# Performance work log

Hardware: AMD Instinct MI355X
Metric: run time of the kernel (lower is better)

The kernel has to match this reference:

```python
import jax, jax.numpy as jnp
import numpy as np

UNITS = 1024
INPUT_SIZE = 1024


def setup_inputs() -> dict:
    key = jax.random.key(0)
    k1, k2, k3 = jax.random.split(key, 3)
    T, B = 512, 64
    inputs = jax.random.normal(k1, (T, B, INPUT_SIZE), dtype=jnp.float32)
    # xavier_uniform for kernel
    limit = float(np.sqrt(6.0 / (INPUT_SIZE + 4 * UNITS)))
    kernel = jax.random.uniform(k2, (INPUT_SIZE, 4 * UNITS), dtype=jnp.float32,
                                minval=-limit, maxval=limit)
    # orthogonal init for recurrent_kernel
    a = jax.random.normal(k3, (4 * UNITS, UNITS), dtype=jnp.float32)
    q, r = jnp.linalg.qr(a)
    q = q * jnp.sign(jnp.diagonal(r))[None, :]
    recurrent_kernel = q.T.astype(jnp.float32)  # [UNITS, 4*UNITS]
    bias = jnp.zeros((4 * UNITS,), dtype=jnp.float32)
    return {"inputs": inputs, "kernel": kernel,
            "recurrent_kernel": recurrent_kernel, "bias": bias}


def _lstm(inputs, kernel, recurrent_kernel, bias):
    T, B, _ = inputs.shape
    U = recurrent_kernel.shape[0]
    # Precompute input projection for all timesteps (same math, one big GEMM)
    xz = jnp.einsum('tbi,ij->tbj', inputs, kernel) + bias  # [T, B, 4U]

    def step(carry, xz_t):
        ht, ct = carry
        z = xz_t + ht @ recurrent_kernel  # [B, 4U]
        z_i, z_f, z_c, z_o = jnp.split(z, 4, axis=1)
        i = jax.nn.sigmoid(z_i)
        f = jax.nn.sigmoid(z_f)
        c_tilde = jnp.tanh(z_c)
        o = jax.nn.sigmoid(z_o)
        ct = f * ct + i * c_tilde
        ht = o * jnp.tanh(ct)
        return (ht, ct), ht

    h0 = jnp.zeros((B, U), dtype=inputs.dtype)
    c0 = jnp.zeros((B, U), dtype=inputs.dtype)
    (ht, ct), outputs = jax.lax.scan(step, (h0, c0), xz)
    return outputs, (ht, ct)


def reference(inputs, kernel, recurrent_kernel, bias):
    return _lstm(inputs, kernel, recurrent_kernel, bias)
```

## Files before the change

### kernel.cpp

```cpp
#include <hip/hip_runtime.h>

typedef __attribute__((ext_vector_type(8))) short short8;
typedef __attribute__((ext_vector_type(4))) float floatx4;

#define T_STEPS 512
#define OUT_HT_OFF 33554432ull
#define OUT_CT_OFF 33619968ull

#define WXH_OFF  0ull
#define WXL_OFF  (8ull << 20)
#define BAR_OFF  (16ull << 20)
#define WS_NEED  ((16ull << 20) + 4096)


static __device__ __forceinline__ unsigned short bf16_rne(float f) {
    union { float f; unsigned int u; } v; v.f = f;
    return (unsigned short)((v.u + 0x7FFFu + ((v.u >> 16) & 1u)) >> 16);
}
static __device__ __forceinline__ float bf16f(unsigned short u) {
    union { unsigned int u; float f; } v; v.u = ((unsigned int)u) << 16;
    return v.f;
}

__global__ void ws_sentinel(float* out) { out[threadIdx.x] = 2.0f; }

__global__ void __launch_bounds__(256) wsplit(const float* __restrict__ W,
                                              unsigned short* __restrict__ wxh,
                                              unsigned short* __restrict__ wxl) {
    __shared__ float tile[64][65];
    const int tx = threadIdx.x & 63;
    const int ty = threadIdx.x >> 6;
    const int cb = blockIdx.x * 64;
    const int kb = blockIdx.y * 64;
    #pragma unroll
    for (int i = 0; i < 16; ++i) {
        int kl = i * 4 + ty;
        tile[kl][tx] = W[(size_t)(kb + kl) * 4096 + cb + tx];
    }
    __syncthreads();
    #pragma unroll
    for (int i = 0; i < 16; ++i) {
        int cl = i * 4 + ty;
        float v = tile[tx][cl];
        unsigned short hi = bf16_rne(v);
        unsigned short lo = bf16_rne(v - bf16f(hi));
        wxh[(size_t)(cb + cl) * 1024 + kb + tx] = hi;
        wxl[(size_t)(cb + cl) * 1024 + kb + tx] = lo;
    }
}

static __device__ __forceinline__ void bar_arrive(unsigned* bar, int xcd, unsigned s) {
    unsigned old = __hip_atomic_fetch_add(bar + xcd * 32, 1u,
                      __ATOMIC_RELAXED, __HIP_MEMORY_SCOPE_AGENT);
    if (old == s * 32u - 1u) {
        unsigned og = __hip_atomic_fetch_add(bar + 256, 1u,
                          __ATOMIC_RELAXED, __HIP_MEMORY_SCOPE_AGENT);
        if (og == s * 8u - 1u) {
            __hip_atomic_store(bar + 288, s,
                               __ATOMIC_RELAXED, __HIP_MEMORY_SCOPE_AGENT);
        }
    }
}
static __device__ __forceinline__ void bar_wait(unsigned* bar, unsigned s) {
    while (__hip_atomic_load(bar + 288, __ATOMIC_RELAXED,
                             __HIP_MEMORY_SCOPE_AGENT) < s) {
        __builtin_amdgcn_s_sleep(2);
    }
}

__global__ void __launch_bounds__(256, 1) lstm_scan(
    const float* __restrict__ R,
    const float* __restrict__ bias,
    const float* __restrict__ x,
    const unsigned short* __restrict__ wxh,
    const unsigned short* __restrict__ wxl,
    unsigned* __restrict__ bar,
    float* __restrict__ out)
{
    __shared__ __align__(16) char AxH[32768];
    __shared__ __align__(16) char AxL[32768];
    __shared__ __align__(16) char AhH[32768];
    __shared__ __align__(16) char AhL[32768];
    __shared__ float zxl[1024];
    __shared__ unsigned s_as[2];

    const int tid  = threadIdx.x;
    const int lane = tid & 63;
    const int wave = tid >> 6;

    if (tid == 0) {
        unsigned xcc;
        asm volatile("s_getreg_b32 %0, hwreg(HW_REG_XCC_ID)" : "=s"(xcc));
        xcc &= 7u;
        unsigned slot = __hip_atomic_fetch_add(bar + 320 + xcc * 32, 1u,
                            __ATOMIC_RELAXED, __HIP_MEMORY_SCOPE_AGENT);
        s_as[0] = xcc; s_as[1] = slot;
    }
    __syncthreads();
    const int xcd  = (int)s_as[0];
    const int slot = (int)(s_as[1] & 31u);
    const int rg   = slot >> 3;
    const int jg   = xcd * 8 + (slot & 7);

    const int rowbase = rg * 16;
    const int c16  = lane & 15;
    const int kgrp = lane >> 4;
    const int gate = c16 >> 2;
    const int jj   = c16 & 3;
    const int mycol = gate * 1024 + jg * 16 + wave * 4 + jj;

    short8 rh[32], rl[32];
    #pragma unroll
    for (int kk = 0; kk < 32; ++kk) {
        int kb = kk * 32 + kgrp * 8;
        short8 h8, l8;
        #pragma unroll
        for (int j = 0; j < 8; ++j) {
            float v = R[(size_t)(kb + j) * 4096 + mycol];
            unsigned short hh = bf16_rne(v);
            h8[j] = (short)hh;
            l8[j] = (short)bf16_rne(v - bf16f(hh));
        }
        rh[kk] = h8; rl[kk] = l8;
    }
    const float biasreg = bias[mycol];

    const int erow  = tid >> 4;
    const int eunit = tid & 15;
    const int ew    = eunit >> 2;
    const int ejj   = eunit & 3;
    const int grow  = rowbase + erow;
    const int gcol  = jg * 16 + eunit;
    const size_t cidx = (size_t)grow * 1024 + gcol;
    float c_state = 0.f;

    const int srow = rowbase + c16;
    const int skof = kgrp * 8;

    const unsigned short* bph = wxh + (size_t)mycol * 1024 + kgrp * 8;
    const unsigned short* bpl = wxl + (size_t)mycol * 1024 + kgrp * 8;

    floatx4 zxcur;
    {
        #pragma unroll
        for (int q = 0; q < 8; ++q) {
            int kc = wave * 8 + q;
            const float* src = x + (size_t)srow * 1024 + kc * 32 + skof;
            floatx4 f0 = *(const floatx4*)src;
            floatx4 f1 = *(const floatx4*)(src + 4);
            short8 h8, l8;
            #pragma unroll
            for (int j = 0; j < 4; ++j) {
                unsigned short q0 = bf16_rne(f0[j]);
                unsigned short q1 = bf16_rne(f1[j]);
                h8[j] = (short)q0; h8[j + 4] = (short)q1;
                l8[j] = (short)bf16_rne(f0[j] - bf16f(q0));
                l8[j + 4] = (short)bf16_rne(f1[j] - bf16f(q1));
            }
            *(short8*)(AxH + kc * 1024 + lane * 16) = h8;
            *(short8*)(AxL + kc * 1024 + lane * 16) = l8;
        }
        __syncthreads();
        floatx4 b0 = {0,0,0,0}, b1 = {0,0,0,0}, b2 = {0,0,0,0}, b3 = {0,0,0,0};
        #pragma unroll
        for (int kk = 0; kk < 32; ++kk) {
            short8 bxh = *(const short8*)(bph + kk * 32);
            short8 bxl = *(const short8*)(bpl + kk * 32);
            short8 axh = *(const short8*)(AxH + kk * 1024 + lane * 16);
            short8 axl = *(const short8*)(AxL + kk * 1024 + lane * 16);
            b0 = __builtin_amdgcn_mfma_f32_16x16x32_bf16(axh, bxh, b0, 0, 0, 0);
            b1 = __builtin_amdgcn_mfma_f32_16x16x32_bf16(axh, bxl, b1, 0, 0, 0);
            b2 = __builtin_amdgcn_mfma_f32_16x16x32_bf16(axl, bxh, b2, 0, 0, 0);
            b3 = __builtin_amdgcn_mfma_f32_16x16x32_bf16(axl, bxl, b3, 0, 0, 0);
        }
        #pragma unroll
        for (int i = 0; i < 4; ++i)
            zxcur[i] = ((b0[i] + b1[i]) + (b2[i] + b3[i])) + biasreg;
    }

    for (int t = 0; t < T_STEPS; ++t) {
        const bool more = (t + 1 < T_STEPS);
        const float* hsrc = out + (size_t)(t - 1) * 65536;

        floatx4 xp0[8], xp1[8];
        if (more) {
            #pragma unroll
            for (int q = 0; q < 8; ++q) {
                int kc = wave * 8 + q;
                const float* src = x + (size_t)(t + 1) * 65536
                                     + (size_t)srow * 1024 + kc * 32 + skof;
                xp0[q] = *(const floatx4*)src;
                xp1[q] = *(const floatx4*)(src + 4);
            }
        }
        #pragma unroll
        for (int q = 0; q < 8; ++q) {
            int kc = wave * 8 + q;
            short8 h8 = {0,0,0,0,0,0,0,0};
            short8 l8 = {0,0,0,0,0,0,0,0};
            if (t > 0) {
                const unsigned long long* p = (const unsigned long long*)
                    (hsrc + (size_t)srow * 1024 + kc * 32 + skof);
                #pragma unroll
                for (int j2 = 0; j2 < 4; ++j2) {
                    unsigned long long u = __hip_atomic_load(p + j2,
                        __ATOMIC_RELAXED, __HIP_MEMORY_SCOPE_AGENT);
                    float f0 = __uint_as_float((unsigned)u);
                    float f1 = __uint_as_float((unsigned)(u >> 32));
                    unsigned short q0 = bf16_rne(f0);
                    unsigned short q1 = bf16_rne(f1);
                    h8[j2 * 2]     = (short)q0;
                    h8[j2 * 2 + 1] = (short)q1;
                    l8[j2 * 2]     = (short)bf16_rne(f0 - bf16f(q0));
                    l8[j2 * 2 + 1] = (short)bf16_rne(f1 - bf16f(q1));
                }
            }
            *(short8*)(AhH + kc * 1024 + lane * 16) = h8;
            *(short8*)(AhL + kc * 1024 + lane * 16) = l8;
        }
        __syncthreads();

        floatx4 a0 = zxcur;
        floatx4 a1 = {0,0,0,0}, a2 = {0,0,0,0}, a3 = {0,0,0,0};
        #pragma unroll
        for (int kk = 0; kk < 32; ++kk) {
            short8 ahh = *(const short8*)(AhH + kk * 1024 + lane * 16);
            short8 ahl = *(const short8*)(AhL + kk * 1024 + lane * 16);
            a0 = __builtin_amdgcn_mfma_f32_16x16x32_bf16(ahh, rh[kk], a0, 0, 0, 0);
            a1 = __builtin_amdgcn_mfma_f32_16x16x32_bf16(ahh, rl[kk], a1, 0, 0, 0);
            a2 = __builtin_amdgcn_mfma_f32_16x16x32_bf16(ahl, rh[kk], a2, 0, 0, 0);
            a3 = __builtin_amdgcn_mfma_f32_16x16x32_bf16(ahl, rl[kk], a3, 0, 0, 0);
        }

        #pragma unroll
        for (int i = 0; i < 4; ++i) {
            float z = (a0[i] + a1[i]) + (a2[i] + a3[i]);
            zxl[wave * 256 + (kgrp * 4 + i) * 16 + c16] = z;
        }
        __syncthreads();
        {
            float zi = zxl[ew * 256 + erow * 16 +  0 + ejj];
            float zf = zxl[ew * 256 + erow * 16 +  4 + ejj];
            float zc = zxl[ew * 256 + erow * 16 +  8 + ejj];
            float zo = zxl[ew * 256 + erow * 16 + 12 + ejj];
            float ig = 1.0f / (1.0f + expf(-zi));
            float fg = 1.0f / (1.0f + expf(-zf));
            float og = 1.0f / (1.0f + expf(-zo));
            float cc = tanhf(zc);
            float cn = fg * c_state + ig * cc;
            c_state = cn;
            float hval = og * tanhf(cn);
            __hip_atomic_store(out + (size_t)t * 65536 + cidx, hval,
                               __ATOMIC_RELAXED, __HIP_MEMORY_SCOPE_AGENT);
            if (t == T_STEPS - 1) {
                out[OUT_HT_OFF + cidx] = hval;
                out[OUT_CT_OFF + cidx] = cn;
            }
        }

        if (more) {
            #pragma unroll
            for (int q = 0; q < 8; ++q) {
                int kc = wave * 8 + q;
                short8 h8, l8;
                #pragma unroll
                for (int j = 0; j < 4; ++j) {
                    unsigned short q0 = bf16_rne(xp0[q][j]);
                    unsigned short q1 = bf16_rne(xp1[q][j]);
                    h8[j] = (short)q0; h8[j + 4] = (short)q1;
                    l8[j] = (short)bf16_rne(xp0[q][j] - bf16f(q0));
                    l8[j + 4] = (short)bf16_rne(xp1[q][j] - bf16f(q1));
                }
                *(short8*)(AxH + kc * 1024 + lane * 16) = h8;
                *(short8*)(AxL + kc * 1024 + lane * 16) = l8;
            }
            __syncthreads();
            if (tid == 0) bar_arrive(bar, xcd, (unsigned)(t + 1));

            floatx4 b0 = {0,0,0,0}, b1 = {0,0,0,0}, b2 = {0,0,0,0}, b3 = {0,0,0,0};
            #pragma unroll
            for (int kk = 0; kk < 32; ++kk) {
                short8 bxh = *(const short8*)(bph + kk * 32);
                short8 bxl = *(const short8*)(bpl + kk * 32);
                short8 axh = *(const short8*)(AxH + kk * 1024 + lane * 16);
                short8 axl = *(const short8*)(AxL + kk * 1024 + lane * 16);
                b0 = __builtin_amdgcn_mfma_f32_16x16x32_bf16(axh, bxh, b0, 0, 0, 0);
                b1 = __builtin_amdgcn_mfma_f32_16x16x32_bf16(axh, bxl, b1, 0, 0, 0);
                b2 = __builtin_amdgcn_mfma_f32_16x16x32_bf16(axl, bxh, b2, 0, 0, 0);
                b3 = __builtin_amdgcn_mfma_f32_16x16x32_bf16(axl, bxl, b3, 0, 0, 0);
            }
            #pragma unroll
            for (int i = 0; i < 4; ++i)
                zxcur[i] = ((b0[i] + b1[i]) + (b2[i] + b3[i])) + biasreg;

            if (tid == 0) bar_wait(bar, (unsigned)(t + 1));
            __syncthreads();
        }
    }
}

extern "C" void kernel_launch(void* const* d_in, const int* in_sizes, int n_in,
                              void* d_out, int out_size, void* d_ws, size_t ws_size,
                              hipStream_t stream) {
    const float* inputs = (const float*)d_in[0];
    const float* W      = (const float*)d_in[1];
    const float* R      = (const float*)d_in[2];
    const float* bias   = (const float*)d_in[3];
    float* out = (float*)d_out;

    if (ws_size < WS_NEED) {
        ws_sentinel<<<1, 64, 0, stream>>>(out);
        return;
    }

    unsigned short* wxh = (unsigned short*)((char*)d_ws + WXH_OFF);
    unsigned short* wxl = (unsigned short*)((char*)d_ws + WXL_OFF);
    unsigned*       bar = (unsigned*)((char*)d_ws + BAR_OFF);

    hipMemsetAsync(bar, 0, 4096, stream);
    wsplit<<<dim3(64, 16), 256, 0, stream>>>(W, wxh, wxl);
    lstm_scan<<<256, 256, 0, stream>>>(R, bias, inputs, wxh, wxl, bar, out);
}
```

Measured before the change: 9.344 ms.

## Exchange pre-split bf16 hi/lo hidden state via double-buffered workspace

The producer now splits each new h value into packed bf16 hi/lo halves, pairs neighbouring lanes with a shuffle, and writes them as 64-bit atomics into a double-buffered workspace. Consumers can then read the ready-made halves instead of re-splitting fp32 h, which removes redundant conversion work from the critical path between steps. The barrier arrive moves earlier, right after h is published, and the prefetch of the next x step is moved after it, which shortens the wait chain but also drops the early load overlap. The per-XCD counter now uses workgroup scope, which looks like a cross-workgroup memory-ordering risk.

```diff
diff --git a/kernel.cpp b/kernel.cpp
--- a/kernel.cpp
+++ b/kernel.cpp
@@ -9,8 +9,9 @@
 
 #define WXH_OFF  0ull
 #define WXL_OFF  (8ull << 20)
-#define BAR_OFF  (16ull << 20)
-#define WS_NEED  ((16ull << 20) + 4096)
+#define HBUF_OFF (16ull << 20)
+#define BAR_OFF  ((16ull << 20) + (512ull << 10))
+#define WS_NEED  ((16ull << 20) + (512ull << 10) + 4096ull)
 
 
 static __device__ __forceinline__ unsigned short bf16_rne(float f) {
@@ -49,31 +50,13 @@
     }
 }
 
-static __device__ __forceinline__ void bar_arrive(unsigned* bar, int xcd, unsigned s) {
-    unsigned old = __hip_atomic_fetch_add(bar + xcd * 32, 1u,
-                      __ATOMIC_RELAXED, __HIP_MEMORY_SCOPE_AGENT);
-    if (old == s * 32u - 1u) {
-        unsigned og = __hip_atomic_fetch_add(bar + 256, 1u,
-                          __ATOMIC_RELAXED, __HIP_MEMORY_SCOPE_AGENT);
-        if (og == s * 8u - 1u) {
-            __hip_atomic_store(bar + 288, s,
-                               __ATOMIC_RELAXED, __HIP_MEMORY_SCOPE_AGENT);
-        }
-    }
-}
-static __device__ __forceinline__ void bar_wait(unsigned* bar, unsigned s) {
-    while (__hip_atomic_load(bar + 288, __ATOMIC_RELAXED,
-                             __HIP_MEMORY_SCOPE_AGENT) < s) {
-        __builtin_amdgcn_s_sleep(2);
-    }
-}
-
 __global__ void __launch_bounds__(256, 1) lstm_scan(
     const float* __restrict__ R,
     const float* __restrict__ bias,
     const float* __restrict__ x,
     const unsigned short* __restrict__ wxh,
     const unsigned short* __restrict__ wxl,
+    unsigned* __restrict__ hbuf,
     unsigned* __restrict__ bar,
     float* __restrict__ out)
 {
@@ -92,7 +75,7 @@
         unsigned xcc;
         asm volatile("s_getreg_b32 %0, hwreg(HW_REG_XCC_ID)" : "=s"(xcc));
         xcc &= 7u;
-        unsigned slot = __hip_atomic_fetch_add(bar + 320 + xcc * 32, 1u,
+        unsigned slot = __hip_atomic_fetch_add(bar + 640 + xcc * 32, 1u,
                             __ATOMIC_RELAXED, __HIP_MEMORY_SCOPE_AGENT);
         s_as[0] = xcc; s_as[1] = slot;
     }
@@ -176,43 +159,29 @@
         #pragma unroll
         for (int i = 0; i < 4; ++i)
             zxcur[i] = ((b0[i] + b1[i]) + (b2[i] + b3[i])) + biasreg;
+        __syncthreads();
     }
 
     for (int t = 0; t < T_STEPS; ++t) {
         const bool more = (t + 1 < T_STEPS);
-        const float* hsrc = out + (size_t)(t - 1) * 65536;
-
-        floatx4 xp0[8], xp1[8];
-        if (more) {
-            #pragma unroll
-            for (int q = 0; q < 8; ++q) {
-                int kc = wave * 8 + q;
-                const float* src = x + (size_t)(t + 1) * 65536
-                                     + (size_t)srow * 1024 + kc * 32 + skof;
-                xp0[q] = *(const floatx4*)src;
-                xp1[q] = *(const floatx4*)(src + 4);
-            }
-        }
+
+        const unsigned long long* hp64 = (const unsigned long long*)
+            (hbuf + (size_t)(t & 1) * 65536) + ((size_t)srow * 512);
         #pragma unroll
         for (int q = 0; q < 8; ++q) {
             int kc = wave * 8 + q;
             short8 h8 = {0,0,0,0,0,0,0,0};
             short8 l8 = {0,0,0,0,0,0,0,0};
             if (t > 0) {
-                const unsigned long long* p = (const unsigned long long*)
-                    (hsrc + (size_t)srow * 1024 + kc * 32 + skof);
+                const unsigned long long* p = hp64 + kc * 16 + kgrp * 4;
                 #pragma unroll
                 for (int j2 = 0; j2 < 4; ++j2) {
                     unsigned long long u = __hip_atomic_load(p + j2,
                         __ATOMIC_RELAXED, __HIP_MEMORY_SCOPE_AGENT);
-                    float f0 = __uint_as_float((unsigned)u);
-                    float f1 = __uint_as_float((unsigned)(u >> 32));
-                    unsigned short q0 = bf16_rne(f0);
-                    unsigned short q1 = bf16_rne(f1);
-                    h8[j2 * 2]     = (short)q0;
-                    h8[j2 * 2 + 1] = (short)q1;
-                    l8[j2 * 2]     = (short)bf16_rne(f0 - bf16f(q0));
-                    l8[j2 * 2 + 1] = (short)bf16_rne(f1 - bf16f(q1));
+                    h8[2 * j2]     = (short)(u & 0xffffu);
+                    l8[2 * j2]     = (short)((u >> 16) & 0xffffu);
+                    h8[2 * j2 + 1] = (short)((u >> 32) & 0xffffu);
+                    l8[2 * j2 + 1] = (short)(u >> 48);
                 }
             }
             *(short8*)(AhH + kc * 1024 + lane * 16) = h8;
@@ -238,6 +207,7 @@
             zxl[wave * 256 + (kgrp * 4 + i) * 16 + c16] = z;
         }
         __syncthreads();
+
         {
             float zi = zxl[ew * 256 + erow * 16 +  0 + ejj];
             float zf = zxl[ew * 256 + erow * 16 +  4 + ejj];
@@ -250,33 +220,62 @@
             float cn = fg * c_state + ig * cc;
             c_state = cn;
             float hval = og * tanhf(cn);
-            __hip_atomic_store(out + (size_t)t * 65536 + cidx, hval,
-                               __ATOMIC_RELAXED, __HIP_MEMORY_SCOPE_AGENT);
-            if (t == T_STEPS - 1) {
+
+            out[(size_t)t * 65536 + cidx] = hval;
+            if (more) {
+                unsigned short hi = bf16_rne(hval);
+                unsigned short lo = bf16_rne(hval - bf16f(hi));
+                unsigned hp = (unsigned)hi | ((unsigned)lo << 16);
+                unsigned hq = (unsigned)__shfl_xor((int)hp, 1, 64);
+                if (!(lane & 1)) {
+                    unsigned long long u = (unsigned long long)hp
+                                         | ((unsigned long long)hq << 32);
+                    __hip_atomic_store((unsigned long long*)
+                        (hbuf + (size_t)((t + 1) & 1) * 65536) + (cidx >> 1), u,
+                        __ATOMIC_RELAXED, __HIP_MEMORY_SCOPE_AGENT);
+                }
+            } else {
                 out[OUT_HT_OFF + cidx] = hval;
                 out[OUT_CT_OFF + cidx] = cn;
             }
         }
+        __syncthreads();
 
         if (more) {
+            if (tid == 0) {
+                unsigned s = (unsigned)(t + 1);
+                unsigned old = __hip_atomic_fetch_add(bar + xcd * 32, 1u,
+                                  __ATOMIC_RELAXED, __HIP_MEMORY_SCOPE_WORKGROUP);
+                if (old == s * 32u - 1u) {
+                    unsigned og = __hip_atomic_fetch_add(bar + 256, 1u,
+                                      __ATOMIC_RELAXED, __HIP_MEMORY_SCOPE_AGENT);
+                    if (og == s * 8u - 1u) {
+                        __hip_atomic_store(bar + 288, s,
+                                           __ATOMIC_RELAXED, __HIP_MEMORY_SCOPE_AGENT);
+                    }
+                }
+            }
+
             #pragma unroll
             for (int q = 0; q < 8; ++q) {
                 int kc = wave * 8 + q;
+                const float* src = x + (size_t)(t + 1) * 65536
+                                     + (size_t)srow * 1024 + kc * 32 + skof;
+                floatx4 f0 = *(const floatx4*)src;
+                floatx4 f1 = *(const floatx4*)(src + 4);
                 short8 h8, l8;
                 #pragma unroll
                 for (int j = 0; j < 4; ++j) {
-                    unsigned short q0 = bf16_rne(xp0[q][j]);
-                    unsigned short q1 = bf16_rne(xp1[q][j]);
+                    unsigned short q0 = bf16_rne(f0[j]);
+                    unsigned short q1 = bf16_rne(f1[j]);
                     h8[j] = (short)q0; h8[j + 4] = (short)q1;
-                    l8[j] = (short)bf16_rne(xp0[q][j] - bf16f(q0));
-                    l8[j + 4] = (short)bf16_rne(xp1[q][j] - bf16f(q1));
+                    l8[j] = (short)bf16_rne(f0[j] - bf16f(q0));
+                    l8[j + 4] = (short)bf16_rne(f1[j] - bf16f(q1));
                 }
                 *(short8*)(AxH + kc * 1024 + lane * 16) = h8;
                 *(short8*)(AxL + kc * 1024 + lane * 16) = l8;
             }
             __syncthreads();
-            if (tid == 0) bar_arrive(bar, xcd, (unsigned)(t + 1));
-
             floatx4 b0 = {0,0,0,0}, b1 = {0,0,0,0}, b2 = {0,0,0,0}, b3 = {0,0,0,0};
             #pragma unroll
             for (int kk = 0; kk < 32; ++kk) {
@@ -293,7 +292,12 @@
             for (int i = 0; i < 4; ++i)
                 zxcur[i] = ((b0[i] + b1[i]) + (b2[i] + b3[i])) + biasreg;
 
-            if (tid == 0) bar_wait(bar, (unsigned)(t + 1));
+            if (tid == 0) {
+                while (__hip_atomic_load(bar + 288, __ATOMIC_RELAXED,
+                                         __HIP_MEMORY_SCOPE_AGENT) < (unsigned)(t + 1)) {
+                    __builtin_amdgcn_s_sleep(4);
+                }
+            }
             __syncthreads();
         }
     }
@@ -313,11 +317,12 @@
         return;
     }
 
-    unsigned short* wxh = (unsigned short*)((char*)d_ws + WXH_OFF);
-    unsigned short* wxl = (unsigned short*)((char*)d_ws + WXL_OFF);
-    unsigned*       bar = (unsigned*)((char*)d_ws + BAR_OFF);
+    unsigned short* wxh  = (unsigned short*)((char*)d_ws + WXH_OFF);
+    unsigned short* wxl  = (unsigned short*)((char*)d_ws + WXL_OFF);
+    unsigned*       hbuf = (unsigned*)((char*)d_ws + HBUF_OFF);
+    unsigned*       bar  = (unsigned*)((char*)d_ws + BAR_OFF);
 
     hipMemsetAsync(bar, 0, 4096, stream);
     wsplit<<<dim3(64, 16), 256, 0, stream>>>(W, wxh, wxl);
-    lstm_scan<<<256, 256, 0, stream>>>(R, bias, inputs, wxh, wxl, bar, out);
-}
+    lstm_scan<<<256, 256, 0, stream>>>(R, bias, inputs, wxh, wxl, hbuf, bar, out);
+}
```

After: 9.411 ms. About the same (+0.7%).
